# Performance work log

Measured on AMD Instinct MI355X. Metric: run time of the kernel, lower is better.

Reference implementation:

```python
import math
import jax, jax.numpy as jnp
import numpy as np

N_NODES = 50000
N_EDGES = 800000
IN_F = 128
OUT_F = 64


def setup_inputs() -> dict:
    key = jax.random.key(0)
    k1, k2, k3, k4 = jax.random.split(key, 4)
    x = jax.random.normal(k1, (N_NODES, IN_F), dtype=jnp.float32)
    edge_index = jax.random.randint(k2, (2, N_EDGES), 0, N_NODES, dtype=jnp.int64)
    # Linear weights, torch layout [out_features, in_features], Kaiming-uniform-like scale
    bound = 1.0 / math.sqrt(IN_F)
    Wq = jax.random.uniform(k3, (OUT_F, IN_F), dtype=jnp.float32, minval=-bound, maxval=bound)
    Wk = jax.random.uniform(k4, (OUT_F, IN_F), dtype=jnp.float32, minval=-bound, maxval=bound)
    return {"x": x, "edge_index": edge_index, "Wq": Wq, "Wk": Wk}


def reference(x, edge_index, Wq, Wk):
    scale = math.sqrt(OUT_F)
    Q = x @ Wq.T  # [N, F]
    K = x @ Wk.T  # [N, F]
    row, col = edge_index[0], edge_index[1]
    # per-edge scaled dot-product attention logits
    alpha = jnp.sum(Q[row] * K[col], axis=-1) / scale  # [E]
    # segment softmax grouped by destination node (col)
    seg_max = jax.ops.segment_max(alpha, col, num_segments=N_NODES)  # [N]
    # empty segments give -inf max; those segments have no edges so exp is never used there
    ex = jnp.exp(alpha - seg_max[col])  # [E]
    denom = jax.ops.segment_sum(ex, col, num_segments=N_NODES)  # [N]
    alpha = ex / (denom[col] + 1e-16)  # [E]
    # dropout p=0 (eval) -> identity
    # weighted scatter-add of source Q features into destination nodes
    out = jax.ops.segment_sum(Q[row] * alpha[:, None], col, num_segments=N_NODES)  # [N, F]
    return out
```

## Files before the change

kernel.cpp:

```cpp
#include <hip/hip_runtime.h>
#include <math.h>

#define N_NODES 50000
#define N_EDGES 800000
#define IN_F 128
#define OUT_F 64

#define NBUK 196
#define BCAP 5120
#define BIN_EPT 8
#define BIN_CHUNK (256 * BIN_EPT)
#define BIN_BLOCKS ((N_EDGES + BIN_CHUNK - 1) / BIN_CHUNK)
#define QK_BLOCKS ((N_NODES + 63) / 64)

typedef __attribute__((ext_vector_type(8))) short short8v;
typedef __attribute__((ext_vector_type(4))) float f32x4;

__device__ __forceinline__ unsigned short bf16_rne(float f) {
    unsigned u = __float_as_uint(f);
    return (unsigned short)((u + 0x7FFFu + ((u >> 16) & 1u)) >> 16);
}
__device__ __forceinline__ void split2(float f, unsigned short& h, unsigned short& l) {
    h = bf16_rne(f);
    float fh = __uint_as_float(((unsigned)h) << 16);
    l = bf16_rne(f - fh);
}
__device__ __forceinline__ float bf2f(ushort h) {
    return __uint_as_float(((unsigned)h) << 16);
}

__global__ __launch_bounds__(256) void wsplit(const float* __restrict__ Wq,
                                              const float* __restrict__ Wk,
                                              ushort* __restrict__ wh,
                                              ushort* __restrict__ wl,
                                              int* __restrict__ bcnt,
                                              int* __restrict__ offs) {
    int i = blockIdx.x * 256 + threadIdx.x;
    if (blockIdx.x == 0 && threadIdx.x < NBUK) bcnt[threadIdx.x] = 0;
    if (blockIdx.x == 0 && threadIdx.x == 0) offs[N_NODES] = N_EDGES;
    if (i >= 2 * OUT_F * IN_F) return;
    float f = (i < OUT_F * IN_F) ? Wq[i] : Wk[i - OUT_F * IN_F];
    unsigned short h, l;
    split2(f, h, l);
    wh[i] = h;
    wl[i] = l;
}

__global__ __launch_bounds__(256) void fat_qk_bin(const float* __restrict__ x,
                                                  const ushort* __restrict__ wh,
                                                  const ushort* __restrict__ wl,
                                                  ushort* __restrict__ Qh,
                                                  ushort* __restrict__ Kh,
                                                  const void* __restrict__ ei,
                                                  int* __restrict__ bcnt,
                                                  unsigned* __restrict__ binned) {
    __shared__ unsigned recbuf[BIN_CHUNK];
    __shared__ int cnt[NBUK];
    __shared__ int gbase[NBUK];
    __shared__ int sflag;
    const int t = threadIdx.x;

    if (blockIdx.x < QK_BLOCKS) {
        const int w = t >> 6, l = t & 63;
        const int base = blockIdx.x * 64 + w * 16;
        const int lr = l & 15, kg = l >> 4;

        int nodeA = base + lr;
        if (nodeA >= N_NODES) nodeA = N_NODES - 1;
        const float* xp = x + (size_t)nodeA * IN_F + kg * 8;

        short8v ah[4], al[4];
#pragma unroll
        for (int ks = 0; ks < 4; ++ks) {
            float4 a0 = *(const float4*)(xp + ks * 32);
            float4 a1 = *(const float4*)(xp + ks * 32 + 4);
            float v[8] = {a0.x, a0.y, a0.z, a0.w, a1.x, a1.y, a1.z, a1.w};
#pragma unroll
            for (int j = 0; j < 8; ++j) {
                unsigned short h, lo;
                split2(v[j], h, lo);
                ah[ks][j] = (short)h;
                al[ks][j] = (short)lo;
            }
        }

#pragma unroll
        for (int mat = 0; mat < 2; ++mat) {
            ushort* O = mat ? Kh : Qh;
            const ushort* whm = wh + mat * (OUT_F * IN_F);
            const ushort* wlm = wl + mat * (OUT_F * IN_F);
#pragma unroll
            for (int nt = 0; nt < 4; ++nt) {
                const int j = nt * 16 + lr;
                const ushort* bhp = whm + (size_t)j * IN_F + kg * 8;
                const ushort* blp = wlm + (size_t)j * IN_F + kg * 8;
                f32x4 acc = {0.0f, 0.0f, 0.0f, 0.0f};
#pragma unroll
                for (int ks = 0; ks < 4; ++ks) {
                    short8v bh = *(const short8v*)(bhp + ks * 32);
                    short8v bl = *(const short8v*)(blp + ks * 32);
                    acc = __builtin_amdgcn_mfma_f32_16x16x32_bf16(ah[ks], bh, acc, 0, 0, 0);
                    acc = __builtin_amdgcn_mfma_f32_16x16x32_bf16(ah[ks], bl, acc, 0, 0, 0);
                    acc = __builtin_amdgcn_mfma_f32_16x16x32_bf16(al[ks], bh, acc, 0, 0, 0);
                }
                const int rowb = base + (l >> 4) * 4;
#pragma unroll
                for (int r = 0; r < 4; ++r) {
                    int node = rowb + r;
                    if (node < N_NODES) O[(size_t)node * OUT_F + j] = bf16_rne(acc[r]);
                }
            }
        }
        return;
    }

    const int bb = blockIdx.x - QK_BLOCKS;
    if (t == 0) {
        const int* p = (const int*)ei;
        int allz = 1;
        for (int i = 0; i < 32; ++i)
            if (p[2 * i + 1] != 0) allz = 0;
        sflag = allz;
    }
    for (int i = t; i < NBUK; i += 256) cnt[i] = 0;
    __syncthreads();

    const int e0 = bb * BIN_CHUNK;
    const int nloc = min(BIN_CHUNK, N_EDGES - e0);
    for (int i = t; i < nloc; i += 256) {
        int e = e0 + i;
        int r, c;
        if (sflag) {
            const long long* p = (const long long*)ei;
            r = (int)p[e];
            c = (int)p[N_EDGES + e];
        } else {
            const int* p = (const int*)ei;
            r = p[e];
            c = p[N_EDGES + e];
        }
        unsigned rec = (unsigned)r | ((unsigned)c << 16);
        recbuf[i] = rec;
        atomicAdd(&cnt[c >> 8], 1);
    }
    __syncthreads();
    for (int i = t; i < NBUK; i += 256) {
        gbase[i] = atomicAdd(&bcnt[i], cnt[i]);
        cnt[i] = 0;
    }
    __syncthreads();
    for (int i = t; i < nloc; i += 256) {
        unsigned rec = recbuf[i];
        int b = rec >> 24;
        int lp = atomicAdd(&cnt[b], 1);
        int pos = gbase[b] + lp;
        if (pos >= BCAP) pos = BCAP - 1;
        binned[(size_t)b * BCAP + pos] = rec;
    }
}

__global__ __launch_bounds__(256) void bucket_build(const unsigned* __restrict__ binned,
                                                    const int* __restrict__ bcnt,
                                                    int* __restrict__ offs,
                                                    ushort* __restrict__ sorted_row) {
    __shared__ int colcnt[256];
    __shared__ int colhead[256];
    __shared__ int s[256];
    __shared__ ushort image[BCAP];
    const int b = blockIdx.x, t = threadIdx.x;
    const int c0 = b << 8;
    const int cntb = bcnt[b];
    const unsigned* slab = binned + (size_t)b * BCAP;

    s[t] = (t < b) ? bcnt[t] : 0;
    __syncthreads();
    for (int off = 128; off > 0; off >>= 1) {
        if (t < off) s[t] += s[t + off];
        __syncthreads();
    }
    const int baseb = s[0];
    __syncthreads();

    colcnt[t] = 0;
    __syncthreads();
    for (int i = t; i < cntb; i += 256)
        atomicAdd(&colcnt[(slab[i] >> 16) & 0xFF], 1);
    __syncthreads();
    s[t] = colcnt[t];
    __syncthreads();
    for (int off = 1; off < 256; off <<= 1) {
        int u = (t >= off) ? s[t - off] : 0;
        __syncthreads();
        s[t] += u;
        __syncthreads();
    }
    const int excl = s[t] - colcnt[t];
    colhead[t] = excl;
    if (c0 + t < N_NODES) offs[c0 + t] = baseb + excl;
    __syncthreads();
    for (int i = t; i < cntb; i += 256) {
        unsigned rec = slab[i];
        int p = atomicAdd(&colhead[(rec >> 16) & 0xFF], 1);
        image[p] = (ushort)(rec & 0xFFFF);
    }
    __syncthreads();
    for (int i = t; i < cntb; i += 256)
        sorted_row[baseb + i] = image[i];
}

__global__ __launch_bounds__(256) void gat_node(const ushort* __restrict__ Qh,
                                                const ushort* __restrict__ Kh,
                                                const ushort* __restrict__ sorted_row,
                                                const int* __restrict__ offs,
                                                float* __restrict__ out) {
    const int wave = threadIdx.x >> 6, lane = threadIdx.x & 63;
    const int n = blockIdx.x * 4 + wave;
    if (n >= N_NODES) return;
    const int g = lane >> 4, gl = lane & 15;
    const int start = offs[n], deg = offs[n + 1] - start;

    const ushort4 kh = *(const ushort4*)(Kh + (size_t)n * OUT_F + gl * 4);
    const float kx = bf2f(kh.x), ky = bf2f(kh.y), kz = bf2f(kh.z), kw = bf2f(kh.w);

    float m0 = -1e30f, d0 = 0.0f;
    float4 o0 = {0.0f, 0.0f, 0.0f, 0.0f};
    float m1 = -1e30f, d1 = 0.0f;
    float4 o1 = {0.0f, 0.0f, 0.0f, 0.0f};

    int i = g;
    for (; i + 4 < deg; i += 8) {
        int r0 = (int)sorted_row[start + i];
        int r1 = (int)sorted_row[start + i + 4];
        ushort4 qh0 = *(const ushort4*)(Qh + (size_t)r0 * OUT_F + gl * 4);
        ushort4 qh1 = *(const ushort4*)(Qh + (size_t)r1 * OUT_F + gl * 4);
        float q0x = bf2f(qh0.x), q0y = bf2f(qh0.y), q0z = bf2f(qh0.z), q0w = bf2f(qh0.w);
        float q1x = bf2f(qh1.x), q1y = bf2f(qh1.y), q1z = bf2f(qh1.z), q1w = bf2f(qh1.w);
        float p0 = q0x * kx + q0y * ky + q0z * kz + q0w * kw;
        float p1 = q1x * kx + q1y * ky + q1z * kz + q1w * kw;
        p0 += __shfl_xor(p0, 1);
        p1 += __shfl_xor(p1, 1);
        p0 += __shfl_xor(p0, 2);
        p1 += __shfl_xor(p1, 2);
        p0 += __shfl_xor(p0, 4);
        p1 += __shfl_xor(p1, 4);
        p0 += __shfl_xor(p0, 8);
        p1 += __shfl_xor(p1, 8);
        p0 *= 0.125f;
        p1 *= 0.125f;
        float mn0 = fmaxf(m0, p0);
        float s0 = __expf(m0 - mn0);
        float e0 = __expf(p0 - mn0);
        d0 = d0 * s0 + e0;
        o0.x = o0.x * s0 + e0 * q0x;
        o0.y = o0.y * s0 + e0 * q0y;
        o0.z = o0.z * s0 + e0 * q0z;
        o0.w = o0.w * s0 + e0 * q0w;
        m0 = mn0;
        float mn1 = fmaxf(m1, p1);
        float s1 = __expf(m1 - mn1);
        float e1 = __expf(p1 - mn1);
        d1 = d1 * s1 + e1;
        o1.x = o1.x * s1 + e1 * q1x;
        o1.y = o1.y * s1 + e1 * q1y;
        o1.z = o1.z * s1 + e1 * q1z;
        o1.w = o1.w * s1 + e1 * q1w;
        m1 = mn1;
    }
    if (i < deg) {
        int r0 = (int)sorted_row[start + i];
        ushort4 qh0 = *(const ushort4*)(Qh + (size_t)r0 * OUT_F + gl * 4);
        float q0x = bf2f(qh0.x), q0y = bf2f(qh0.y), q0z = bf2f(qh0.z), q0w = bf2f(qh0.w);
        float p0 = q0x * kx + q0y * ky + q0z * kz + q0w * kw;
        p0 += __shfl_xor(p0, 1);
        p0 += __shfl_xor(p0, 2);
        p0 += __shfl_xor(p0, 4);
        p0 += __shfl_xor(p0, 8);
        p0 *= 0.125f;
        float mn0 = fmaxf(m0, p0);
        float s0 = __expf(m0 - mn0);
        float e0 = __expf(p0 - mn0);
        d0 = d0 * s0 + e0;
        o0.x = o0.x * s0 + e0 * q0x;
        o0.y = o0.y * s0 + e0 * q0y;
        o0.z = o0.z * s0 + e0 * q0z;
        o0.w = o0.w * s0 + e0 * q0w;
        m0 = mn0;
    }

    {
        float mn = fmaxf(m0, m1);
        float s0 = __expf(m0 - mn);
        float s1 = __expf(m1 - mn);
        d0 = d0 * s0 + d1 * s1;
        o0.x = o0.x * s0 + o1.x * s1;
        o0.y = o0.y * s0 + o1.y * s1;
        o0.z = o0.z * s0 + o1.z * s1;
        o0.w = o0.w * s0 + o1.w * s1;
        m0 = mn;
    }

#pragma unroll
    for (int off = 16; off <= 32; off <<= 1) {
        float m2 = __shfl_xor(m0, off);
        float d2 = __shfl_xor(d0, off);
        float ox = __shfl_xor(o0.x, off);
        float oy = __shfl_xor(o0.y, off);
        float oz = __shfl_xor(o0.z, off);
        float ow = __shfl_xor(o0.w, off);
        float mn = fmaxf(m0, m2);
        float s1 = __expf(m0 - mn);
        float s2 = __expf(m2 - mn);
        d0 = d0 * s1 + d2 * s2;
        o0.x = o0.x * s1 + ox * s2;
        o0.y = o0.y * s1 + oy * s2;
        o0.z = o0.z * s1 + oz * s2;
        o0.w = o0.w * s1 + ow * s2;
        m0 = mn;
    }

    if (g == 0) {
        float inv = 1.0f / (d0 + 1e-16f);
        float4 r = {o0.x * inv, o0.y * inv, o0.z * inv, o0.w * inv};
        *(float4*)(out + (size_t)n * OUT_F + gl * 4) = r;
    }
}

extern "C" void kernel_launch(void* const* d_in, const int* in_sizes, int n_in,
                              void* d_out, int out_size, void* d_ws, size_t ws_size,
                              hipStream_t stream) {
    const float* x = (const float*)d_in[0];
    const void* ei = d_in[1];
    const float* Wq = (const float*)d_in[2];
    const float* Wk = (const float*)d_in[3];
    float* out = (float*)d_out;

    char* ws = (char*)d_ws;
    ushort* Qh = (ushort*)ws;         ws += (size_t)N_NODES * OUT_F * 2;
    ushort* Kh = (ushort*)ws;         ws += (size_t)N_NODES * OUT_F * 2;
    unsigned* binned = (unsigned*)ws; ws += (size_t)NBUK * BCAP * 4;
    ushort* sorted_row = (ushort*)ws; ws += (size_t)N_EDGES * 2;
    ushort* wh = (ushort*)ws;         ws += (size_t)2 * OUT_F * IN_F * 2;
    ushort* wl = (ushort*)ws;         ws += (size_t)2 * OUT_F * IN_F * 2;
    ws = (char*)(((size_t)ws + 255) & ~(size_t)255);
    int* bcnt = (int*)ws;             ws += (size_t)NBUK * 4;
    int* offs = (int*)ws;             ws += (size_t)(N_NODES + 1) * 4;

    wsplit<<<(2 * OUT_F * IN_F + 255) / 256, 256, 0, stream>>>(Wq, Wk, wh, wl, bcnt, offs);
    fat_qk_bin<<<QK_BLOCKS + BIN_BLOCKS, 256, 0, stream>>>(x, wh, wl, Qh, Kh, ei, bcnt, binned);
    bucket_build<<<NBUK, 256, 0, stream>>>(binned, bcnt, offs, sorted_row);
    gat_node<<<(N_NODES + 3) / 4, 256, 0, stream>>>(Qh, Kh, sorted_row, offs, out);
}
```

Baseline: 91.20 us.

## Split fused QK/binning kernel and stage split weights in swizzled LDS

The combined QK-projection and edge-binning kernel becomes two separate launches. The new QK kernel copies the bf16 hi/lo weight splits for both matrices (64 KB) into LDS with an XOR swizzle, instead of reading them from global memory or cache on every MFMA step. This aims to cut redundant weight traffic, and the swizzle is meant to avoid LDS bank conflicts. In exchange it adds an extra kernel launch, loses the overlap between binning and the GEMM inside one grid, and lowers occupancy because of the large LDS footprint.

```diff
diff --git a/kernel.cpp b/kernel.cpp
--- a/kernel.cpp
+++ b/kernel.cpp
@@ -11,7 +11,8 @@
 #define BIN_EPT 8
 #define BIN_CHUNK (256 * BIN_EPT)
 #define BIN_BLOCKS ((N_EDGES + BIN_CHUNK - 1) / BIN_CHUNK)
-#define QK_BLOCKS ((N_NODES + 63) / 64)
+#define QK_NB 64
+#define QK_BLOCKS ((N_NODES + QK_NB - 1) / QK_NB)
 
 typedef __attribute__((ext_vector_type(8))) short short8v;
 typedef __attribute__((ext_vector_type(4))) float f32x4;
@@ -46,75 +47,14 @@
     wl[i] = l;
 }
 
-__global__ __launch_bounds__(256) void fat_qk_bin(const float* __restrict__ x,
-                                                  const ushort* __restrict__ wh,
-                                                  const ushort* __restrict__ wl,
-                                                  ushort* __restrict__ Qh,
-                                                  ushort* __restrict__ Kh,
-                                                  const void* __restrict__ ei,
-                                                  int* __restrict__ bcnt,
-                                                  unsigned* __restrict__ binned) {
+__global__ __launch_bounds__(256) void bin_edges(const void* __restrict__ ei,
+                                                 int* __restrict__ bcnt,
+                                                 unsigned* __restrict__ binned) {
     __shared__ unsigned recbuf[BIN_CHUNK];
     __shared__ int cnt[NBUK];
     __shared__ int gbase[NBUK];
     __shared__ int sflag;
     const int t = threadIdx.x;
-
-    if (blockIdx.x < QK_BLOCKS) {
-        const int w = t >> 6, l = t & 63;
-        const int base = blockIdx.x * 64 + w * 16;
-        const int lr = l & 15, kg = l >> 4;
-
-        int nodeA = base + lr;
-        if (nodeA >= N_NODES) nodeA = N_NODES - 1;
-        const float* xp = x + (size_t)nodeA * IN_F + kg * 8;
-
-        short8v ah[4], al[4];
-#pragma unroll
-        for (int ks = 0; ks < 4; ++ks) {
-            float4 a0 = *(const float4*)(xp + ks * 32);
-            float4 a1 = *(const float4*)(xp + ks * 32 + 4);
-            float v[8] = {a0.x, a0.y, a0.z, a0.w, a1.x, a1.y, a1.z, a1.w};
-#pragma unroll
-            for (int j = 0; j < 8; ++j) {
-                unsigned short h, lo;
-                split2(v[j], h, lo);
-                ah[ks][j] = (short)h;
-                al[ks][j] = (short)lo;
-            }
-        }
-
-#pragma unroll
-        for (int mat = 0; mat < 2; ++mat) {
-            ushort* O = mat ? Kh : Qh;
-            const ushort* whm = wh + mat * (OUT_F * IN_F);
-            const ushort* wlm = wl + mat * (OUT_F * IN_F);
-#pragma unroll
-            for (int nt = 0; nt < 4; ++nt) {
-                const int j = nt * 16 + lr;
-                const ushort* bhp = whm + (size_t)j * IN_F + kg * 8;
-                const ushort* blp = wlm + (size_t)j * IN_F + kg * 8;
-                f32x4 acc = {0.0f, 0.0f, 0.0f, 0.0f};
-#pragma unroll
-                for (int ks = 0; ks < 4; ++ks) {
-                    short8v bh = *(const short8v*)(bhp + ks * 32);
-                    short8v bl = *(const short8v*)(blp + ks * 32);
-                    acc = __builtin_amdgcn_mfma_f32_16x16x32_bf16(ah[ks], bh, acc, 0, 0, 0);
-                    acc = __builtin_amdgcn_mfma_f32_16x16x32_bf16(ah[ks], bl, acc, 0, 0, 0);
-                    acc = __builtin_amdgcn_mfma_f32_16x16x32_bf16(al[ks], bh, acc, 0, 0, 0);
-                }
-                const int rowb = base + (l >> 4) * 4;
-#pragma unroll
-                for (int r = 0; r < 4; ++r) {
-                    int node = rowb + r;
-                    if (node < N_NODES) O[(size_t)node * OUT_F + j] = bf16_rne(acc[r]);
-                }
-            }
-        }
-        return;
-    }
-
-    const int bb = blockIdx.x - QK_BLOCKS;
     if (t == 0) {
         const int* p = (const int*)ei;
         int allz = 1;
@@ -125,7 +65,7 @@
     for (int i = t; i < NBUK; i += 256) cnt[i] = 0;
     __syncthreads();
 
-    const int e0 = bb * BIN_CHUNK;
+    const int e0 = blockIdx.x * BIN_CHUNK;
     const int nloc = min(BIN_CHUNK, N_EDGES - e0);
     for (int i = t; i < nloc; i += 256) {
         int e = e0 + i;
@@ -206,6 +146,80 @@
     __syncthreads();
     for (int i = t; i < cntb; i += 256)
         sorted_row[baseb + i] = image[i];
+}
+
+__global__ __launch_bounds__(256, 2) void qk_mfma(const float* __restrict__ x,
+                                                  const ushort* __restrict__ wh,
+                                                  const ushort* __restrict__ wl,
+                                                  ushort* __restrict__ Qh,
+                                                  ushort* __restrict__ Kh) {
+    __shared__ ushort blds[4 * 64 * 128];
+    char* lds0 = (char*)&blds[0];
+    const int t = threadIdx.x;
+
+    for (int u = t; u < 4096; u += 256) {
+        int mh = u >> 10;
+        int j = (u >> 4) & 63;
+        int kb = u & 15;
+        const ushort* src = (mh & 1) ? wl : wh;
+        int soff = ((mh >> 1) << 13) + (j << 7) + (kb << 3);
+        short8v v = *(const short8v*)(src + soff);
+        unsigned byte = ((unsigned)u * 16u) ^ (((unsigned)j & 7u) << 4);
+        *(short8v*)(lds0 + byte) = v;
+    }
+
+    const int w = t >> 6, l = t & 63;
+    const int base = blockIdx.x * QK_NB + w * 16;
+    const int lr = l & 15, kg = l >> 4;
+
+    int nodeA = base + lr;
+    if (nodeA >= N_NODES) nodeA = N_NODES - 1;
+    const float* xp = x + (size_t)nodeA * IN_F + kg * 8;
+
+    short8v ah[4], al[4];
+#pragma unroll
+    for (int ks = 0; ks < 4; ++ks) {
+        float4 a0 = *(const float4*)(xp + ks * 32);
+        float4 a1 = *(const float4*)(xp + ks * 32 + 4);
+        float v[8] = {a0.x, a0.y, a0.z, a0.w, a1.x, a1.y, a1.z, a1.w};
+#pragma unroll
+        for (int jj = 0; jj < 8; ++jj) {
+            unsigned short h, lo;
+            split2(v[jj], h, lo);
+            ah[ks][jj] = (short)h;
+            al[ks][jj] = (short)lo;
+        }
+    }
+
+    __syncthreads();
+
+#pragma unroll
+    for (int mat = 0; mat < 2; ++mat) {
+        ushort* O = mat ? Kh : Qh;
+#pragma unroll
+        for (int nt = 0; nt < 4; ++nt) {
+            const int j = nt * 16 + lr;
+            const unsigned swz = (((unsigned)j & 7u) << 4);
+            const unsigned bh_base = (unsigned)((mat * 2 + 0) * 64 + j) * 256u;
+            const unsigned bl_base = (unsigned)((mat * 2 + 1) * 64 + j) * 256u;
+            f32x4 acc = {0.0f, 0.0f, 0.0f, 0.0f};
+#pragma unroll
+            for (int ks = 0; ks < 4; ++ks) {
+                unsigned off = ((unsigned)kg << 4) + ((unsigned)ks << 6);
+                short8v bh = *(const short8v*)(lds0 + ((bh_base + off) ^ swz));
+                short8v bl = *(const short8v*)(lds0 + ((bl_base + off) ^ swz));
+                acc = __builtin_amdgcn_mfma_f32_16x16x32_bf16(ah[ks], bh, acc, 0, 0, 0);
+                acc = __builtin_amdgcn_mfma_f32_16x16x32_bf16(ah[ks], bl, acc, 0, 0, 0);
+                acc = __builtin_amdgcn_mfma_f32_16x16x32_bf16(al[ks], bh, acc, 0, 0, 0);
+            }
+            const int rowb = base + kg * 4;
+#pragma unroll
+            for (int r = 0; r < 4; ++r) {
+                int node = rowb + r;
+                if (node < N_NODES) O[(size_t)node * OUT_F + j] = bf16_rne(acc[r]);
+            }
+        }
+    }
 }
 
 __global__ __launch_bounds__(256) void gat_node(const ushort* __restrict__ Qh,
@@ -346,7 +360,8 @@
     int* offs = (int*)ws;             ws += (size_t)(N_NODES + 1) * 4;
 
     wsplit<<<(2 * OUT_F * IN_F + 255) / 256, 256, 0, stream>>>(Wq, Wk, wh, wl, bcnt, offs);
-    fat_qk_bin<<<QK_BLOCKS + BIN_BLOCKS, 256, 0, stream>>>(x, wh, wl, Qh, Kh, ei, bcnt, binned);
+    bin_edges<<<BIN_BLOCKS, 256, 0, stream>>>(ei, bcnt, binned);
+    qk_mfma<<<QK_BLOCKS, 256, 0, stream>>>(x, wh, wl, Qh, Kh);
     bucket_build<<<NBUK, 256, 0, stream>>>(binned, bcnt, offs, sorted_row);
     gat_node<<<(N_NODES + 3) / 4, 256, 0, stream>>>(Qh, Kh, sorted_row, offs, out);
 }
```

After: 85.70 us. -6.0%, faster.
